# Kernel optimization log

Measured on AMD Instinct MI355X. Metric: run time of the kernel, lower is better.

## Reference

```python
import jax, jax.numpy as jnp
import numpy as np

B, A, E = 16384, 8, 512


def setup_inputs() -> dict:
    key = jax.random.key(0)
    ks = jax.random.split(key, 6)
    return {
        "image_features": jax.random.normal(ks[0], (B, E), dtype=jnp.float32),
        "edge_attributes": jax.random.normal(ks[1], (B, A, E), dtype=jnp.float32),
        "linear_w": jax.random.normal(ks[2], (E, 2 * E), dtype=jnp.float32) * (1.0 / np.sqrt(2 * E)),
        "linear_b": jax.random.normal(ks[3], (E,), dtype=jnp.float32) * 0.01,
        "fwd_proj": jax.random.normal(ks[4], (A, E, E), dtype=jnp.float32) * (1.0 / np.sqrt(E)),
        "bwd_proj": jax.random.normal(ks[5], (A, E, E), dtype=jnp.float32) * (1.0 / np.sqrt(E)),
        "self_weighted": jnp.ones((1, A, 1), dtype=jnp.float32),
    }


def reference(image_features, edge_attributes, linear_w, linear_b, fwd_proj, bwd_proj, self_weighted):
    # Forward attribute GNN: broadcast src over attribute axis, concat, linear(2E->E)
    src = jnp.broadcast_to(image_features[:, None, :], edge_attributes.shape)  # [B,A,E]
    x = jnp.concatenate([src, edge_attributes], axis=-1)                       # [B,A,2E]
    agg = jnp.einsum('bak,ek->bae', x, linear_w) + linear_b                    # [B,A,E]
    attr_rep = jnp.einsum('bai,aij->baj', agg, fwd_proj)                       # [B,A,E]

    # Backward attribute GNN: per-type projection, ReLU, learned weighted sum over A
    proj = jnp.einsum('bai,aij->baj', attr_rep, bwd_proj)                      # [B,A,E]
    individuals = jnp.sum(jax.nn.relu(proj) * self_weighted, axis=1)           # [B,E]
    return attr_rep, individuals
```

## Files before the change

kernel.cpp:

```cpp
#include <hip/hip_runtime.h>
#include <cstdint>
#include <cstddef>

#define NB 16384
#define NA 8
#define NE 512
#define NK 1024
#define NN 4096

typedef __bf16 bf16x8 __attribute__((ext_vector_type(8)));
typedef float  f32x4  __attribute__((ext_vector_type(4)));
typedef uint16_t u16x8 __attribute__((ext_vector_type(8)));

__device__ __forceinline__ uint16_t cvt_bf16(float f) {
    uint32_t u = __builtin_bit_cast(uint32_t, f);
    u += 0x7fffu + ((u >> 16) & 1u);
    return (uint16_t)(u >> 16);
}

__device__ __forceinline__ int swz(int row) { return (row ^ (row >> 2)) & 3; }

__device__ __forceinline__ void gl_lds16(const void* g, void* l) {
    __builtin_amdgcn_global_load_lds(
        (__attribute__((address_space(1))) void*)(void*)g,
        (__attribute__((address_space(3))) void*)l, 16, 0, 0);
}

__global__ __launch_bounds__(256) void k_tcvt(const float* __restrict__ in,
                                              uint16_t* __restrict__ out,
                                              int R, int C) {
    __shared__ float tile[32][33];
    int mat = blockIdx.z;
    int c0 = blockIdx.x * 32, r0 = blockIdx.y * 32;
    int tx = threadIdx.x & 31, ty = threadIdx.x >> 5;
    const float* src = in + (size_t)mat * R * C;
    uint16_t* dst = out + (size_t)mat * R * C;
#pragma unroll
    for (int yy = 0; yy < 4; ++yy) {
        int r = ty + yy * 8;
        tile[r][tx] = src[(size_t)(r0 + r) * C + c0 + tx];
    }
    __syncthreads();
#pragma unroll
    for (int yy = 0; yy < 4; ++yy) {
        int c = ty + yy * 8;
        dst[(size_t)(c0 + c) * R + r0 + tx] = cvt_bf16(tile[tx][c]);
    }
}

__global__ __launch_bounds__(256) void k_cvt4(const float* __restrict__ in,
                                              uint16_t* __restrict__ out, int n4) {
    int i = blockIdx.x * 256 + threadIdx.x;
    if (i >= n4) return;
    float4 v = ((const float4*)in)[i];
    ushort4 o;
    o.x = cvt_bf16(v.x); o.y = cvt_bf16(v.y); o.z = cvt_bf16(v.z); o.w = cvt_bf16(v.w);
    ((ushort4*)out)[i] = o;
}

__global__ __launch_bounds__(256) void k_bvec(const float* __restrict__ lb,
                                              const float* __restrict__ fwd,
                                              float* __restrict__ bvec) {
    int a = blockIdx.x >> 4, i0 = (blockIdx.x & 15) * 32;
    int t = threadIdx.x;
    float s0 = 0.f, s1 = 0.f;
#pragma unroll 4
    for (int i = 0; i < 32; ++i) {
        float w = lb[i0 + i];
        const float* f = fwd + ((size_t)a * NE + i0 + i) * NE;
        s0 = fmaf(w, f[t], s0);
        s1 = fmaf(w, f[t + 256], s1);
    }
    atomicAdd(&bvec[a * NE + t], s0);
    atomicAdd(&bvec[a * NE + t + 256], s1);
}

__global__ __launch_bounds__(256) void k_prep(const uint16_t* __restrict__ lwT,
                                              const uint16_t* __restrict__ fwdT,
                                              uint16_t* __restrict__ TMT) {
    __shared__ alignas(16) uint16_t lA[128 * 32];
    __shared__ alignas(16) uint16_t lB[128 * 32];
    int bz = blockIdx.x;
    int nt = bz & 31, mt = bz >> 5;
    int m0 = mt * 128, n0 = nt * 128;
    int t = threadIdx.x, lane = t & 63;
    int w = t >> 6, wm = w >> 1, wn = w & 1;
    int lr = lane & 15, lc = lane >> 4;
    int sl = swz(lr);
    f32x4 acc[4][4] = {};
    for (int k0 = 0; k0 < NE; k0 += 32) {
        __syncthreads();
#pragma unroll
        for (int p = 0; p < 2; ++p) {
            int idx = p * 256 + t;
            int row = idx >> 2, c16 = (idx & 3) ^ swz(row);
            gl_lds16(lwT + (size_t)(m0 + row) * NE + k0 + c16 * 8, lA + idx * 8);
            gl_lds16(fwdT + (size_t)(n0 + row) * NE + k0 + c16 * 8, lB + idx * 8);
        }
        __syncthreads();
        bf16x8 af[4], bfr[4];
#pragma unroll
        for (int i = 0; i < 4; ++i)
            af[i] = *(const bf16x8*)&lA[(wm * 64 + i * 16 + lr) * 32 + ((lc ^ sl) << 3)];
#pragma unroll
        for (int j = 0; j < 4; ++j)
            bfr[j] = *(const bf16x8*)&lB[(wn * 64 + j * 16 + lr) * 32 + ((lc ^ sl) << 3)];
#pragma unroll
        for (int i = 0; i < 4; ++i)
#pragma unroll
            for (int j = 0; j < 4; ++j)
                acc[i][j] = __builtin_amdgcn_mfma_f32_16x16x32_bf16(af[i], bfr[j], acc[i][j], 0, 0, 0);
    }
#pragma unroll
    for (int i = 0; i < 4; ++i) {
        int mb = m0 + wm * 64 + i * 16 + lc * 4;
#pragma unroll
        for (int j = 0; j < 4; ++j) {
            int n = n0 + wn * 64 + j * 16 + lr;
            ushort4 v;
            v.x = cvt_bf16(acc[i][j][0]);
            v.y = cvt_bf16(acc[i][j][1]);
            v.z = cvt_bf16(acc[i][j][2]);
            v.w = cvt_bf16(acc[i][j][3]);
            *(ushort4*)&TMT[(size_t)n * NK + mb] = v;
        }
    }
}

template<bool EDGEB, bool WB>
__global__ __launch_bounds__(256) void k_mm(const uint16_t* __restrict__ imgb,
                                            const float* __restrict__ edgef,
                                            const uint16_t* __restrict__ edgeb,
                                            const uint16_t* __restrict__ TMT,
                                            const float* __restrict__ bvec,
                                            float* __restrict__ attr,
                                            uint16_t* __restrict__ attrb) {
    __shared__ alignas(16) uint16_t lA[128 * 64];
    __shared__ alignas(16) uint16_t lB[128 * 64];
    int bz = blockIdx.x;
    int nt = bz & 31, mt = bz >> 5;
    int a = nt >> 2, jt = nt & 3;
    int m0 = mt * 128, jb = jt * 128;
    int t = threadIdx.x, lane = t & 63;
    int w = t >> 6, wm = w >> 1, wn = w & 1;
    int lr = lane & 15, lc = lane >> 4;
    f32x4 acc[4][4];
#pragma unroll
    for (int j = 0; j < 4; ++j) {
        float bv = bvec[a * NE + jb + wn * 64 + j * 16 + lr];
        f32x4 b4 = {bv, bv, bv, bv};
#pragma unroll
        for (int i = 0; i < 4; ++i) acc[i][j] = b4;
    }
    for (int k0 = 0; k0 < NK; k0 += 64) {
        __syncthreads();
        if (k0 < NE) {
#pragma unroll
            for (int p = 0; p < 4; ++p) {
                int idx = p * 256 + t;
                int row = idx >> 3, cg = (idx & 7) ^ (row & 7);
                gl_lds16(imgb + (size_t)(m0 + row) * NE + k0 + cg * 8, lA + idx * 8);
            }
        } else if (EDGEB) {
#pragma unroll
            for (int p = 0; p < 4; ++p) {
                int idx = p * 256 + t;
                int row = idx >> 3, cg = (idx & 7) ^ (row & 7);
                gl_lds16(edgeb + ((size_t)(m0 + row) * NA + a) * NE + (k0 - NE) + cg * 8, lA + idx * 8);
            }
        } else {
#pragma unroll
            for (int p = 0; p < 4; ++p) {
                int idx = p * 256 + t;
                int row = idx >> 3, c = idx & 7, cg = c ^ (row & 7);
                const float* s = edgef + ((size_t)(m0 + row) * NA + a) * NE + (k0 - NE) + c * 8;
                float4 v0 = ((const float4*)s)[0];
                float4 v1 = ((const float4*)s)[1];
                u16x8 o = {cvt_bf16(v0.x), cvt_bf16(v0.y), cvt_bf16(v0.z), cvt_bf16(v0.w),
                           cvt_bf16(v1.x), cvt_bf16(v1.y), cvt_bf16(v1.z), cvt_bf16(v1.w)};
                *(u16x8*)&lA[row * 64 + cg * 8] = o;
            }
        }
#pragma unroll
        for (int p = 0; p < 4; ++p) {
            int idx = p * 256 + t;
            int row = idx >> 3, cg = (idx & 7) ^ (row & 7);
            gl_lds16(TMT + (size_t)(a * NE + jb + row) * NK + k0 + cg * 8, lB + idx * 8);
        }
        __syncthreads();
#pragma unroll
        for (int h = 0; h < 2; ++h) {
            bf16x8 af[4], bfr[4];
#pragma unroll
            for (int i = 0; i < 4; ++i)
                af[i] = *(const bf16x8*)&lA[(wm * 64 + i * 16 + lr) * 64 + (((h * 4 + lc) ^ (lr & 7)) << 3)];
#pragma unroll
            for (int j = 0; j < 4; ++j)
                bfr[j] = *(const bf16x8*)&lB[(wn * 64 + j * 16 + lr) * 64 + (((h * 4 + lc) ^ (lr & 7)) << 3)];
#pragma unroll
            for (int i = 0; i < 4; ++i)
#pragma unroll
                for (int j = 0; j < 4; ++j)
                    acc[i][j] = __builtin_amdgcn_mfma_f32_16x16x32_bf16(af[i], bfr[j], acc[i][j], 0, 0, 0);
        }
    }
#pragma unroll
    for (int i = 0; i < 4; ++i) {
#pragma unroll
        for (int r = 0; r < 4; ++r) {
            int bm = m0 + wm * 64 + i * 16 + lc * 4 + r;
            float* orow = attr + ((size_t)bm * NA + a) * NE + jb;
#pragma unroll
            for (int j = 0; j < 4; ++j)
                orow[wn * 64 + j * 16 + lr] = acc[i][j][r];
            if (WB) {
                uint16_t* brow = attrb + ((size_t)bm * NA + a) * NE + jb;
#pragma unroll
                for (int j = 0; j < 4; ++j)
                    brow[wn * 64 + j * 16 + lr] = cvt_bf16(acc[i][j][r]);
            }
        }
    }
}

template<bool AB>
__global__ __launch_bounds__(256) void k_ind2(const float* __restrict__ attrf,
                                              const uint16_t* __restrict__ attrb,
                                              const uint16_t* __restrict__ bwdT,
                                              const float* __restrict__ sw,
                                              float* __restrict__ ind) {
    __shared__ alignas(16) uint16_t lA[128 * 64];
    __shared__ alignas(16) uint16_t lB[128 * 64];
    int bz = blockIdx.x;
    int jt = bz & 3, mt = bz >> 2;
    int m0 = mt * 128, jb = jt * 128;
    int t = threadIdx.x, lane = t & 63;
    int w = t >> 6, wm = w >> 1, wn = w & 1;
    int lr = lane & 15, lc = lane >> 4;
    f32x4 res[4][4] = {};
    for (int a = 0; a < NA; ++a) {
        float wa = sw[a];
        f32x4 acc[4][4] = {};
        for (int k0 = 0; k0 < NE; k0 += 64) {
            __syncthreads();
            if (AB) {
#pragma unroll
                for (int p = 0; p < 4; ++p) {
                    int idx = p * 256 + t;
                    int row = idx >> 3, cg = (idx & 7) ^ (row & 7);
                    gl_lds16(attrb + ((size_t)(m0 + row) * NA + a) * NE + k0 + cg * 8, lA + idx * 8);
                }
            } else {
#pragma unroll
                for (int p = 0; p < 4; ++p) {
                    int idx = p * 256 + t;
                    int row = idx >> 3, c = idx & 7, cg = c ^ (row & 7);
                    const float* s = attrf + ((size_t)(m0 + row) * NA + a) * NE + k0 + c * 8;
                    float4 v0 = ((const float4*)s)[0];
                    float4 v1 = ((const float4*)s)[1];
                    u16x8 o = {cvt_bf16(v0.x), cvt_bf16(v0.y), cvt_bf16(v0.z), cvt_bf16(v0.w),
                               cvt_bf16(v1.x), cvt_bf16(v1.y), cvt_bf16(v1.z), cvt_bf16(v1.w)};
                    *(u16x8*)&lA[row * 64 + cg * 8] = o;
                }
            }
#pragma unroll
            for (int p = 0; p < 4; ++p) {
                int idx = p * 256 + t;
                int row = idx >> 3, cg = (idx & 7) ^ (row & 7);
                gl_lds16(bwdT + (size_t)(a * NE + jb + row) * NE + k0 + cg * 8, lB + idx * 8);
            }
            __syncthreads();
#pragma unroll
            for (int h = 0; h < 2; ++h) {
                bf16x8 af[4], bfr[4];
#pragma unroll
                for (int i = 0; i < 4; ++i)
                    af[i] = *(const bf16x8*)&lA[(wm * 64 + i * 16 + lr) * 64 + (((h * 4 + lc) ^ (lr & 7)) << 3)];
#pragma unroll
                for (int j = 0; j < 4; ++j)
                    bfr[j] = *(const bf16x8*)&lB[(wn * 64 + j * 16 + lr) * 64 + (((h * 4 + lc) ^ (lr & 7)) << 3)];
#pragma unroll
                for (int i = 0; i < 4; ++i)
#pragma unroll
                    for (int j = 0; j < 4; ++j)
                        acc[i][j] = __builtin_amdgcn_mfma_f32_16x16x32_bf16(af[i], bfr[j], acc[i][j], 0, 0, 0);
            }
        }
#pragma unroll
        for (int i = 0; i < 4; ++i)
#pragma unroll
            for (int j = 0; j < 4; ++j)
#pragma unroll
                for (int r = 0; r < 4; ++r)
                    res[i][j][r] += wa * fmaxf(acc[i][j][r], 0.f);
    }
#pragma unroll
    for (int i = 0; i < 4; ++i) {
#pragma unroll
        for (int r = 0; r < 4; ++r) {
            int bm = m0 + wm * 64 + i * 16 + lc * 4 + r;
            float* orow = ind + (size_t)bm * NE + jb;
#pragma unroll
            for (int j = 0; j < 4; ++j)
                orow[wn * 64 + j * 16 + lr] = res[i][j][r];
        }
    }
}

extern "C" void kernel_launch(void* const* d_in, const int* in_sizes, int n_in,
                              void* d_out, int out_size, void* d_ws, size_t ws_size,
                              hipStream_t stream) {
    (void)in_sizes; (void)n_in; (void)out_size;
    const float* img  = (const float*)d_in[0];
    const float* edge = (const float*)d_in[1];
    const float* lw   = (const float*)d_in[2];
    const float* lb   = (const float*)d_in[3];
    const float* fwd  = (const float*)d_in[4];
    const float* bwd  = (const float*)d_in[5];
    const float* sw   = (const float*)d_in[6];
    float* attr = (float*)d_out;
    float* ind  = attr + (size_t)NB * NA * NE;

    char* ws = (char*)d_ws;
    size_t off = 0;
    auto alloc = [&](size_t bytes) { void* p = ws + off; off += bytes; return p; };
    uint16_t* lwT  = (uint16_t*)alloc((size_t)NK * NE * 2);
    uint16_t* fwdT = (uint16_t*)alloc((size_t)NA * NE * NE * 2);
    uint16_t* bwdT = (uint16_t*)alloc((size_t)NA * NE * NE * 2);
    uint16_t* TMT  = (uint16_t*)alloc((size_t)NN * NK * 2);
    uint16_t* imgb = (uint16_t*)alloc((size_t)NB * NE * 2);
    float*    bvec = (float*)alloc((size_t)NN * 4);

    const size_t BIGB = (size_t)NB * NA * NE * 2;
    bool has_attrb = ws_size >= off + BIGB;
    uint16_t* attrb = has_attrb ? (uint16_t*)alloc(BIGB) : (uint16_t*)0;
    bool has_edgeb = ws_size >= off + BIGB;
    uint16_t* edgeb = has_edgeb ? (uint16_t*)alloc(BIGB) : (uint16_t*)0;

    hipMemsetAsync(bvec, 0, (size_t)NN * 4, stream);
    k_tcvt<<<dim3(NK / 32, NE / 32, 1), 256, 0, stream>>>(lw, lwT, NE, NK);
    k_tcvt<<<dim3(NE / 32, NE / 32, NA), 256, 0, stream>>>(fwd, fwdT, NE, NE);
    k_tcvt<<<dim3(NE / 32, NE / 32, NA), 256, 0, stream>>>(bwd, bwdT, NE, NE);
    k_cvt4<<<NB * NE / 4 / 256, 256, 0, stream>>>(img, imgb, NB * NE / 4);
    if (has_edgeb)
        k_cvt4<<<NB * NA * NE / 4 / 256, 256, 0, stream>>>(edge, edgeb, NB * NA * NE / 4);
    k_bvec<<<128, 256, 0, stream>>>(lb, fwd, bvec);
    k_prep<<<(NK / 128) * (NN / 128), 256, 0, stream>>>(lwT, fwdT, TMT);

    int mm_grid = (NB / 128) * (NN / 128);
    if (has_edgeb && has_attrb)
        k_mm<true, true><<<mm_grid, 256, 0, stream>>>(imgb, edge, edgeb, TMT, bvec, attr, attrb);
    else if (has_edgeb)
        k_mm<true, false><<<mm_grid, 256, 0, stream>>>(imgb, edge, edgeb, TMT, bvec, attr, attrb);
    else if (has_attrb)
        k_mm<false, true><<<mm_grid, 256, 0, stream>>>(imgb, edge, edgeb, TMT, bvec, attr, attrb);
    else
        k_mm<false, false><<<mm_grid, 256, 0, stream>>>(imgb, edge, edgeb, TMT, bvec, attr, attrb);

    int ind_grid = (NB / 128) * (NE / 128);
    if (has_attrb)
        k_ind2<true><<<ind_grid, 256, 0, stream>>>(attr, attrb, bwdT, sw, ind);
    else
        k_ind2<false><<<ind_grid, 256, 0, stream>>>(attr, attrb, bwdT, sw, ind);
}
```

Measured before the change: 534.4 us.

## Double-buffer GEMM LDS tiles, remap blocks per XCD, split ind kernel over attributes

Both GEMM kernels now use double-buffered LDS tiles with a K-step of 32. The next stage's global-to-LDS load is issued before the current tile's MFMAs, so one barrier per step replaces two. Block indices are remapped so each XCD handles one attribute type (k_mm) or one j-tile and attribute half (k_ind2), which is meant to improve L2 reuse of weight tiles. k_ind2 doubles its grid by splitting the 8 attributes into two halves whose partial sums are combined with float atomicAdd into a zero-initialised output. This adds a memset and atomic traffic and makes the summation order nondeterministic.

```diff
diff --git a/kernel.cpp b/kernel.cpp
--- a/kernel.cpp
+++ b/kernel.cpp
@@ -135,15 +135,23 @@
                                             const float* __restrict__ bvec,
                                             float* __restrict__ attr,
                                             uint16_t* __restrict__ attrb) {
-    __shared__ alignas(16) uint16_t lA[128 * 64];
-    __shared__ alignas(16) uint16_t lB[128 * 64];
-    int bz = blockIdx.x;
-    int nt = bz & 31, mt = bz >> 5;
-    int a = nt >> 2, jt = nt & 3;
+    __shared__ alignas(16) uint16_t lA[2][128 * 32];
+    __shared__ alignas(16) uint16_t lB[2][128 * 32];
+    int o = blockIdx.x;
+    int xcd = o & 7, idx = o >> 3;
+    int a = xcd, jt = idx & 3, mt = idx >> 2;
     int m0 = mt * 128, jb = jt * 128;
     int t = threadIdx.x, lane = t & 63;
     int w = t >> 6, wm = w >> 1, wn = w & 1;
     int lr = lane & 15, lc = lane >> 4;
+    int sl = swz(lr);
+    int srow[2], scol[2];
+#pragma unroll
+    for (int p = 0; p < 2; ++p) {
+        int id = p * 256 + t;
+        srow[p] = id >> 2;
+        scol[p] = ((id & 3) ^ swz(id >> 2)) << 3;
+    }
     f32x4 acc[4][4];
 #pragma unroll
     for (int j = 0; j < 4; ++j) {
@@ -152,57 +160,52 @@
 #pragma unroll
         for (int i = 0; i < 4; ++i) acc[i][j] = b4;
     }
-    for (int k0 = 0; k0 < NK; k0 += 64) {
+    auto stage = [&](int buf, int s) {
+        int k0 = s * 32;
+        if (k0 < NE) {
+#pragma unroll
+            for (int p = 0; p < 2; ++p)
+                gl_lds16(imgb + (size_t)(m0 + srow[p]) * NE + k0 + scol[p],
+                         &lA[buf][(p * 256 + t) * 8]);
+        } else if (EDGEB) {
+#pragma unroll
+            for (int p = 0; p < 2; ++p)
+                gl_lds16(edgeb + ((size_t)(m0 + srow[p]) * NA + a) * NE + (k0 - NE) + scol[p],
+                         &lA[buf][(p * 256 + t) * 8]);
+        } else {
+#pragma unroll
+            for (int p = 0; p < 2; ++p) {
+                const float* sp = edgef + ((size_t)(m0 + srow[p]) * NA + a) * NE + (k0 - NE) + scol[p];
+                float4 v0 = ((const float4*)sp)[0];
+                float4 v1 = ((const float4*)sp)[1];
+                u16x8 ov = {cvt_bf16(v0.x), cvt_bf16(v0.y), cvt_bf16(v0.z), cvt_bf16(v0.w),
+                            cvt_bf16(v1.x), cvt_bf16(v1.y), cvt_bf16(v1.z), cvt_bf16(v1.w)};
+                *(u16x8*)&lA[buf][(p * 256 + t) * 8] = ov;
+            }
+        }
+#pragma unroll
+        for (int p = 0; p < 2; ++p)
+            gl_lds16(TMT + (size_t)(a * NE + jb + srow[p]) * NK + k0 + scol[p],
+                     &lB[buf][(p * 256 + t) * 8]);
+    };
+    stage(0, 0);
+    __syncthreads();
+    for (int s = 0; s < 32; ++s) {
+        int cur = s & 1;
+        if (s + 1 < 32) stage(cur ^ 1, s + 1);
+        bf16x8 af[4], bfr[4];
+#pragma unroll
+        for (int i = 0; i < 4; ++i)
+            af[i] = *(const bf16x8*)&lA[cur][(wm * 64 + i * 16 + lr) * 32 + ((lc ^ sl) << 3)];
+#pragma unroll
+        for (int j = 0; j < 4; ++j)
+            bfr[j] = *(const bf16x8*)&lB[cur][(wn * 64 + j * 16 + lr) * 32 + ((lc ^ sl) << 3)];
+#pragma unroll
+        for (int i = 0; i < 4; ++i)
+#pragma unroll
+            for (int j = 0; j < 4; ++j)
+                acc[i][j] = __builtin_amdgcn_mfma_f32_16x16x32_bf16(af[i], bfr[j], acc[i][j], 0, 0, 0);
         __syncthreads();
-        if (k0 < NE) {
-#pragma unroll
-            for (int p = 0; p < 4; ++p) {
-                int idx = p * 256 + t;
-                int row = idx >> 3, cg = (idx & 7) ^ (row & 7);
-                gl_lds16(imgb + (size_t)(m0 + row) * NE + k0 + cg * 8, lA + idx * 8);
-            }
-        } else if (EDGEB) {
-#pragma unroll
-            for (int p = 0; p < 4; ++p) {
-                int idx = p * 256 + t;
-                int row = idx >> 3, cg = (idx & 7) ^ (row & 7);
-                gl_lds16(edgeb + ((size_t)(m0 + row) * NA + a) * NE + (k0 - NE) + cg * 8, lA + idx * 8);
-            }
-        } else {
-#pragma unroll
-            for (int p = 0; p < 4; ++p) {
-                int idx = p * 256 + t;
-                int row = idx >> 3, c = idx & 7, cg = c ^ (row & 7);
-                const float* s = edgef + ((size_t)(m0 + row) * NA + a) * NE + (k0 - NE) + c * 8;
-                float4 v0 = ((const float4*)s)[0];
-                float4 v1 = ((const float4*)s)[1];
-                u16x8 o = {cvt_bf16(v0.x), cvt_bf16(v0.y), cvt_bf16(v0.z), cvt_bf16(v0.w),
-                           cvt_bf16(v1.x), cvt_bf16(v1.y), cvt_bf16(v1.z), cvt_bf16(v1.w)};
-                *(u16x8*)&lA[row * 64 + cg * 8] = o;
-            }
-        }
-#pragma unroll
-        for (int p = 0; p < 4; ++p) {
-            int idx = p * 256 + t;
-            int row = idx >> 3, cg = (idx & 7) ^ (row & 7);
-            gl_lds16(TMT + (size_t)(a * NE + jb + row) * NK + k0 + cg * 8, lB + idx * 8);
-        }
-        __syncthreads();
-#pragma unroll
-        for (int h = 0; h < 2; ++h) {
-            bf16x8 af[4], bfr[4];
-#pragma unroll
-            for (int i = 0; i < 4; ++i)
-                af[i] = *(const bf16x8*)&lA[(wm * 64 + i * 16 + lr) * 64 + (((h * 4 + lc) ^ (lr & 7)) << 3)];
-#pragma unroll
-            for (int j = 0; j < 4; ++j)
-                bfr[j] = *(const bf16x8*)&lB[(wn * 64 + j * 16 + lr) * 64 + (((h * 4 + lc) ^ (lr & 7)) << 3)];
-#pragma unroll
-            for (int i = 0; i < 4; ++i)
-#pragma unroll
-                for (int j = 0; j < 4; ++j)
-                    acc[i][j] = __builtin_amdgcn_mfma_f32_16x16x32_bf16(af[i], bfr[j], acc[i][j], 0, 0, 0);
-        }
     }
 #pragma unroll
     for (int i = 0; i < 4; ++i) {
@@ -229,70 +232,78 @@
                                               const uint16_t* __restrict__ bwdT,
                                               const float* __restrict__ sw,
                                               float* __restrict__ ind) {
-    __shared__ alignas(16) uint16_t lA[128 * 64];
-    __shared__ alignas(16) uint16_t lB[128 * 64];
-    int bz = blockIdx.x;
-    int jt = bz & 3, mt = bz >> 2;
-    int m0 = mt * 128, jb = jt * 128;
+    __shared__ alignas(16) uint16_t lA[2][128 * 32];
+    __shared__ alignas(16) uint16_t lB[2][128 * 32];
+    int o = blockIdx.x;
+    int xcd = o & 7, mt = o >> 3;
+    int jt = xcd >> 1, ah = xcd & 1;
+    int m0 = mt * 128, jb = jt * 128, a0 = ah * 4;
     int t = threadIdx.x, lane = t & 63;
     int w = t >> 6, wm = w >> 1, wn = w & 1;
     int lr = lane & 15, lc = lane >> 4;
+    int sl = swz(lr);
+    int srow[2], scol[2];
+#pragma unroll
+    for (int p = 0; p < 2; ++p) {
+        int id = p * 256 + t;
+        srow[p] = id >> 2;
+        scol[p] = ((id & 3) ^ swz(id >> 2)) << 3;
+    }
     f32x4 res[4][4] = {};
-    for (int a = 0; a < NA; ++a) {
-        float wa = sw[a];
-        f32x4 acc[4][4] = {};
-        for (int k0 = 0; k0 < NE; k0 += 64) {
-            __syncthreads();
-            if (AB) {
-#pragma unroll
-                for (int p = 0; p < 4; ++p) {
-                    int idx = p * 256 + t;
-                    int row = idx >> 3, cg = (idx & 7) ^ (row & 7);
-                    gl_lds16(attrb + ((size_t)(m0 + row) * NA + a) * NE + k0 + cg * 8, lA + idx * 8);
+    f32x4 acc[4][4] = {};
+    auto stage = [&](int buf, int s) {
+        int a = a0 + (s >> 4), kk = (s & 15) * 32;
+        if (AB) {
+#pragma unroll
+            for (int p = 0; p < 2; ++p)
+                gl_lds16(attrb + ((size_t)(m0 + srow[p]) * NA + a) * NE + kk + scol[p],
+                         &lA[buf][(p * 256 + t) * 8]);
+        } else {
+#pragma unroll
+            for (int p = 0; p < 2; ++p) {
+                const float* sp = attrf + ((size_t)(m0 + srow[p]) * NA + a) * NE + kk + scol[p];
+                float4 v0 = ((const float4*)sp)[0];
+                float4 v1 = ((const float4*)sp)[1];
+                u16x8 ov = {cvt_bf16(v0.x), cvt_bf16(v0.y), cvt_bf16(v0.z), cvt_bf16(v0.w),
+                            cvt_bf16(v1.x), cvt_bf16(v1.y), cvt_bf16(v1.z), cvt_bf16(v1.w)};
+                *(u16x8*)&lA[buf][(p * 256 + t) * 8] = ov;
+            }
+        }
+#pragma unroll
+        for (int p = 0; p < 2; ++p)
+            gl_lds16(bwdT + (size_t)(a * NE + jb + srow[p]) * NE + kk + scol[p],
+                     &lB[buf][(p * 256 + t) * 8]);
+    };
+    stage(0, 0);
+    __syncthreads();
+    for (int s = 0; s < 64; ++s) {
+        int cur = s & 1;
+        if (s + 1 < 64) stage(cur ^ 1, s + 1);
+        bf16x8 af[4], bfr[4];
+#pragma unroll
+        for (int i = 0; i < 4; ++i)
+            af[i] = *(const bf16x8*)&lA[cur][(wm * 64 + i * 16 + lr) * 32 + ((lc ^ sl) << 3)];
+#pragma unroll
+        for (int j = 0; j < 4; ++j)
+            bfr[j] = *(const bf16x8*)&lB[cur][(wn * 64 + j * 16 + lr) * 32 + ((lc ^ sl) << 3)];
+#pragma unroll
+        for (int i = 0; i < 4; ++i)
+#pragma unroll
+            for (int j = 0; j < 4; ++j)
+                acc[i][j] = __builtin_amdgcn_mfma_f32_16x16x32_bf16(af[i], bfr[j], acc[i][j], 0, 0, 0);
+        if ((s & 15) == 15) {
+            float wa = sw[a0 + (s >> 4)];
+#pragma unroll
+            for (int i = 0; i < 4; ++i)
+#pragma unroll
+                for (int j = 0; j < 4; ++j) {
+#pragma unroll
+                    for (int r = 0; r < 4; ++r)
+                        res[i][j][r] += wa * fmaxf(acc[i][j][r], 0.f);
+                    acc[i][j] = (f32x4){0.f, 0.f, 0.f, 0.f};
                 }
-            } else {
-#pragma unroll
-                for (int p = 0; p < 4; ++p) {
-                    int idx = p * 256 + t;
-                    int row = idx >> 3, c = idx & 7, cg = c ^ (row & 7);
-                    const float* s = attrf + ((size_t)(m0 + row) * NA + a) * NE + k0 + c * 8;
-                    float4 v0 = ((const float4*)s)[0];
-                    float4 v1 = ((const float4*)s)[1];
-                    u16x8 o = {cvt_bf16(v0.x), cvt_bf16(v0.y), cvt_bf16(v0.z), cvt_bf16(v0.w),
-                               cvt_bf16(v1.x), cvt_bf16(v1.y), cvt_bf16(v1.z), cvt_bf16(v1.w)};
-                    *(u16x8*)&lA[row * 64 + cg * 8] = o;
-                }
-            }
-#pragma unroll
-            for (int p = 0; p < 4; ++p) {
-                int idx = p * 256 + t;
-                int row = idx >> 3, cg = (idx & 7) ^ (row & 7);
-                gl_lds16(bwdT + (size_t)(a * NE + jb + row) * NE + k0 + cg * 8, lB + idx * 8);
-            }
-            __syncthreads();
-#pragma unroll
-            for (int h = 0; h < 2; ++h) {
-                bf16x8 af[4], bfr[4];
-#pragma unroll
-                for (int i = 0; i < 4; ++i)
-                    af[i] = *(const bf16x8*)&lA[(wm * 64 + i * 16 + lr) * 64 + (((h * 4 + lc) ^ (lr & 7)) << 3)];
-#pragma unroll
-                for (int j = 0; j < 4; ++j)
-                    bfr[j] = *(const bf16x8*)&lB[(wn * 64 + j * 16 + lr) * 64 + (((h * 4 + lc) ^ (lr & 7)) << 3)];
-#pragma unroll
-                for (int i = 0; i < 4; ++i)
-#pragma unroll
-                    for (int j = 0; j < 4; ++j)
-                        acc[i][j] = __builtin_amdgcn_mfma_f32_16x16x32_bf16(af[i], bfr[j], acc[i][j], 0, 0, 0);
-            }
-        }
-#pragma unroll
-        for (int i = 0; i < 4; ++i)
-#pragma unroll
-            for (int j = 0; j < 4; ++j)
-#pragma unroll
-                for (int r = 0; r < 4; ++r)
-                    res[i][j][r] += wa * fmaxf(acc[i][j][r], 0.f);
+        }
+        __syncthreads();
     }
 #pragma unroll
     for (int i = 0; i < 4; ++i) {
@@ -302,7 +313,7 @@
             float* orow = ind + (size_t)bm * NE + jb;
 #pragma unroll
             for (int j = 0; j < 4; ++j)
-                orow[wn * 64 + j * 16 + lr] = res[i][j][r];
+                atomicAdd(&orow[wn * 64 + j * 16 + lr], res[i][j][r]);
         }
     }
 }
@@ -338,6 +349,7 @@
     uint16_t* edgeb = has_edgeb ? (uint16_t*)alloc(BIGB) : (uint16_t*)0;
 
     hipMemsetAsync(bvec, 0, (size_t)NN * 4, stream);
+    hipMemsetAsync(ind, 0, (size_t)NB * NE * 4, stream);
     k_tcvt<<<dim3(NK / 32, NE / 32, 1), 256, 0, stream>>>(lw, lwT, NE, NK);
     k_tcvt<<<dim3(NE / 32, NE / 32, NA), 256, 0, stream>>>(fwd, fwdT, NE, NE);
     k_tcvt<<<dim3(NE / 32, NE / 32, NA), 256, 0, stream>>>(bwd, bwdT, NE, NE);
@@ -357,7 +369,7 @@
     else
         k_mm<false, false><<<mm_grid, 256, 0, stream>>>(imgb, edge, edgeb, TMT, bvec, attr, attrb);
 
-    int ind_grid = (NB / 128) * (NE / 128);
+    int ind_grid = (NB / 128) * (NE / 128) * 2;
     if (has_attrb)
         k_ind2<true><<<ind_grid, 256, 0, stream>>>(attr, attrb, bwdT, sw, ind);
     else
```

After: 511.2 us. 4.3% less time.
